# Optimization experiments

Measured on AMD Instinct MI355X. Metric: run time of the kernel, lower is better.

Reference implementation:

```python
import jax, jax.numpy as jnp
import numpy as np
from jax import lax

NPIX = 256        # charge grid size
OS = 3            # oversample / stride
KS = 9            # dynamic kernel window size (3 * OS)
TIME_STEPS = 8
ORDER = 2

# polynomial powers: all (px, py) with px + py <= ORDER, shape (2, n_terms)
_pairs = [(i, s - i) for s in range(ORDER + 1) for i in range(s + 1)]
POWERS = jnp.asarray(np.array(_pairs).T, dtype=jnp.float32)  # (2, 6)
NTERMS = POWERS.shape[1]
NFEAT = 2 * NTERMS  # 12 encoder output channels


def pixel_coords(n, diameter):
    # dLux-style pixel center coordinates, shape (2, n, n)
    pitch = diameter / n
    c = ((jnp.arange(n) - (n - 1) / 2.0) * pitch).astype(jnp.float32)
    return jnp.stack(jnp.meshgrid(c, c, indexing="ij"))


def downsample(x, n, mean):
    h, w = x.shape
    r = x.reshape(h // n, n, w // n, n)
    return r.mean((1, 3)) if mean else r.sum((1, 3))


def conv2d_same(x, w):
    # x: (C, H, W), w: (O, C, 3, 3), SAME padding, no bias
    return lax.conv_general_dilated(
        x[None], w, (1, 1), "SAME",
        dimension_numbers=("NCHW", "OIHW", "NCHW"))[0]


def calc_kernels(coords):
    # coords: (npix, npix, 2, 3, 3) distorted sub-pixel centers
    npix = coords.shape[0]
    # full[c, 3i+p, 3j+q] = coords[i, j, c, p, q]  (kernels_to_array over both channels)
    full = coords.transpose(2, 0, 3, 1, 4).reshape(2, OS * npix, OS * npix)
    pc31 = pixel_coords(3, 1.0)                      # (2, 3, 3)
    empty = jnp.tile(pc31, (1, npix + 2, npix + 2))  # (2, 3(npix+2), 3(npix+2))
    padded = empty.at[:, 3:-3, 3:-3].set(full)
    rel = jnp.repeat(jnp.repeat(pixel_coords(3, 3.0), 3, axis=1), 3, axis=2)  # (2, 9, 9)
    win = jnp.stack([
        jnp.stack([padded[:, u:u + 3 * npix - 2:3, v:v + 3 * npix - 2:3]
                   for v in range(KS)], axis=1)
        for u in range(KS)], axis=1)                 # (2, 9, 9, npix, npix)
    x = win[0] + rel[0][..., None, None]
    y = win[1] + rel[1][..., None, None]
    size = jnp.float32(1.0 / 3.0)
    # overlap of a size x size box at (x, y) with the unit box centered at 0
    ox = jnp.maximum(0.0, jnp.minimum(x + size / 2, 0.5) - jnp.maximum(x - size / 2, -0.5))
    oy = jnp.maximum(0.0, jnp.minimum(y + size / 2, 0.5) - jnp.maximum(y - size / 2, -0.5))
    frac = ox * oy / (size * size)                   # (9, 9, npix, npix)
    return frac.transpose(2, 3, 0, 1)                # (npix, npix, 9, 9)


def dfn_kernels(charge, w1, w2, w3):
    # encoder: conv(1->32) relu conv(32->32) relu conv(32->12)
    f = jax.nn.relu(conv2d_same(charge[None], w1))
    f = jax.nn.relu(conv2d_same(f, w2))
    f = conv2d_same(f, w3)                           # (12, npix, npix)
    npix = charge.shape[-1]
    coeffs = f.reshape(2, NTERMS, npix, npix)        # per-pixel (2, n_terms)
    knots = pixel_coords(3, 1.0)                     # (2, 3, 3)
    pow_base = (knots[0][None] ** POWERS[0][:, None, None]) * \
               (knots[1][None] ** POWERS[1][:, None, None])   # (n_terms, 3, 3)
    distortion = jnp.einsum("ctij,txy->ijcxy", coeffs, pow_base)
    coords = knots[None, None] + distortion          # (npix, npix, 2, 3, 3)
    return calc_kernels(coords)


def apply_kernels_stride(illum, kernels):
    # illum: (3*npix, 3*npix); kernels: (npix, npix, 9, 9)
    npix = kernels.shape[0]
    pad = KS // OS  # 3
    ip = jnp.pad(illum, pad)
    out = jnp.zeros((npix, npix), illum.dtype)
    for u in range(KS):          # fixed 9x9 offset loop, each iter fully vectorized
        for v in range(KS):
            out = out + ip[u:u + 3 * npix - 2:3, v:v + 3 * npix - 2:3] * kernels[:, :, u, v]
    return out


def setup_inputs() -> dict:
    key = jax.random.key(0)
    ks = jax.random.split(key, 6)
    return {
        "bias": jax.random.normal(ks[0], (NPIX, NPIX), jnp.float32),
        "illuminance": jax.random.uniform(ks[1], (3 * NPIX, 3 * NPIX), jnp.float32),
        "sensitivity": jax.random.uniform(ks[2], (3 * NPIX, 3 * NPIX), jnp.float32),
        "w1": 0.05 * jax.random.normal(ks[3], (32, 1, 3, 3), jnp.float32),
        "w2": 0.05 * jax.random.normal(ks[4], (32, 32, 3, 3), jnp.float32),
        "w3": 0.05 * jax.random.normal(ks[5], (NFEAT, 32, 3, 3), jnp.float32),
    }


def reference(bias, illuminance, sensitivity, w1, w2, w3):
    illum_full = illuminance / TIME_STEPS
    illum = downsample(sensitivity * illum_full, OS, mean=False)   # (npix, npix)
    sens = downsample(sensitivity, OS, mean=True)                  # (npix, npix)
    charge = bias - jnp.mean(bias)                                 # use_bias=True
    charges = [charge]
    diffusions = []
    for _ in range(TIME_STEPS):  # bleed=True path
        norm_charge = charge - jnp.mean(charge)
        kernels = dfn_kernels(norm_charge, w1, w2, w3)
        new_charge = sens * apply_kernels_stride(illum_full, kernels)
        charge = charge + new_charge
        diffusions.append(illum - new_charge)
        charges.append(charge)
    ramp = jnp.stack(charges) + jnp.median(bias)                   # (T+1, npix, npix)
    return ramp, jnp.stack(diffusions)                             # (T, npix, npix)
```

## Files before the change

kernel.cpp:

```cpp
#include <hip/hip_runtime.h>

#define N2 65536
#define FW 768

#define WS_CHARGE 0
#define WS_ILLUM  (N2)
#define WS_SENS   (2*N2)
#define WS_FEAT2  (3*N2)
#define WS_W1T    (35*N2)
#define WS_W2T    (WS_W1T + 288)
#define WS_W3T    (WS_W2T + 9216)
#define WS_SUMS   (WS_W3T + 3456)
#define WS_BSUM   (WS_SUMS + 9)
#define WS_MEANB  (WS_SUMS + 10)
#define WS_MEDIAN (WS_SUMS + 11)
#define WS_SEL    (WS_SUMS + 12)
#define WS_H2     (WS_SUMS + 16)
#define WS_H3     (WS_H2 + 2048)
#define NCLEAR    (16 + 2048 + 2048)
#define WS_H1     (WS_H3 + 2048)

__device__ __forceinline__ void block_sum_atomic(float v, float* dst){
  #pragma unroll
  for (int o = 32; o > 0; o >>= 1) v += __shfl_down(v, o, 64);
  __shared__ float red[16];
  int lane = threadIdx.x & 63, wid = threadIdx.x >> 6;
  int nw = (int)(blockDim.x >> 6);
  if (lane == 0) red[wid] = v;
  __syncthreads();
  if (threadIdx.x == 0){
    float s = red[0];
    for (int w = 1; w < nw; w++) s += red[w];
    atomicAdd(dst, s);
  }
}

__device__ __forceinline__ unsigned block_scan_u32(unsigned v, unsigned* wsum){
  __syncthreads();
  int lane = threadIdx.x & 63, wid = threadIdx.x >> 6, nw = (int)(blockDim.x >> 6);
  unsigned x = v;
  #pragma unroll
  for (int o = 1; o < 64; o <<= 1){ unsigned y = __shfl_up(x, o, 64); if (lane >= o) x += y; }
  if (lane == 63) wsum[wid] = x;
  __syncthreads();
  if (wid == 0){
    unsigned w = (lane < nw) ? wsum[lane] : 0u;
    #pragma unroll
    for (int o = 1; o < 16; o <<= 1){ unsigned y = __shfl_up(w, o, 64); if (lane >= o) w += y; }
    if (lane < nw) wsum[lane] = w;
  }
  __syncthreads();
  unsigned base = (wid > 0) ? wsum[wid - 1] : 0u;
  return base + x;
}

__device__ __forceinline__ unsigned key_flip(unsigned u){
  return (u & 0x80000000u) ? ~u : (u ^ 0x80000000u);
}

__global__ __launch_bounds__(256) void k_prep(const float* __restrict__ w1,
    const float* __restrict__ w2, const float* __restrict__ w3,
    float* __restrict__ ws){
  int t = blockIdx.x * 256 + threadIdx.x;
  unsigned* z = (unsigned*)(ws + WS_SUMS);
  for (int i = t; i < NCLEAR; i += 2048) z[i] = 0u;
  for (int idx = t; idx < 288; idx += 2048){
    int co = idx / 9, k = idx - co*9;
    ws[WS_W1T + k*32 + co] = w1[idx];
  }
  for (int idx = t; idx < 9216; idx += 2048){
    int co = idx / 288, r = idx - co*288, ci = r / 9, k = r - ci*9;
    ws[WS_W2T + (ci*9 + k)*32 + co] = w2[idx];
  }
  for (int idx = t; idx < 3456; idx += 2048){
    int co = idx / 288, r = idx - co*288, ci = r / 9, k = r - ci*9;
    ws[WS_W3T + (ci*9 + k)*12 + co] = w3[idx];
  }
}

__global__ __launch_bounds__(256) void k_h1(const float* __restrict__ bias,
                                            float* __restrict__ ws){
  __shared__ unsigned h[4096];
  for (int i = threadIdx.x; i < 4096; i += 256) h[i] = 0u;
  __syncthreads();
  float s = 0.f;
  for (int i = blockIdx.x * 256 + threadIdx.x; i < N2; i += 32*256){
    float v = bias[i]; s += v;
    atomicAdd(&h[key_flip(__float_as_uint(v)) >> 20], 1u);
  }
  __syncthreads();
  unsigned* H1 = (unsigned*)(ws + WS_H1) + (blockIdx.x << 12);
  for (int i = threadIdx.x; i < 4096; i += 256) H1[i] = h[i];
  block_sum_atomic(s, ws + WS_BSUM);
}

__global__ __launch_bounds__(1024) void k_s1(float* __restrict__ ws){
  const unsigned* H1 = (const unsigned*)(ws + WS_H1);
  unsigned* sel = (unsigned*)(ws + WS_SEL);
  __shared__ unsigned wssc[16];
  int t = threadIdx.x;
  uint4 hv = make_uint4(0u, 0u, 0u, 0u);
  for (int b = 0; b < 32; b++){
    uint4 v = ((const uint4*)(H1 + (b << 12)))[t];
    hv.x += v.x; hv.y += v.y; hv.z += v.z; hv.w += v.w;
  }
  unsigned c4 = hv.x + hv.y + hv.z + hv.w;
  unsigned cum = block_scan_u32(c4, wssc);
  unsigned before = cum - c4;
  unsigned hh[4] = {hv.x, hv.y, hv.z, hv.w};
  for (int s = 0; s < 2; s++){
    unsigned rank = 32767u + (unsigned)s;
    if (before <= rank && rank < cum){
      unsigned kk = rank - before, acc = 0; unsigned b = 0;
      for (; b < 3; b++){ if (acc + hh[b] > kk) break; acc += hh[b]; }
      sel[s]     = 4u*(unsigned)t + b;
      sel[2 + s] = kk - acc;
    }
  }
  if (t == 0) ws[WS_MEANB] = ws[WS_BSUM] * (1.f / (float)N2);
}

__global__ __launch_bounds__(256) void k_h23(const float* __restrict__ bias,
    float* __restrict__ ws, unsigned* __restrict__ H, int shift){
  const unsigned* sel = (const unsigned*)(ws + WS_SEL);
  unsigned p0 = sel[0], p1 = sel[1];
  for (int i = blockIdx.x * 256 + threadIdx.x; i < N2; i += 64*256){
    unsigned key = key_flip(__float_as_uint(bias[i]));
    unsigned top = key >> (shift + 10);
    unsigned bin = (key >> shift) & 1023u;
    if (top == p0) atomicAdd(&H[bin], 1u);
    if (top == p1) atomicAdd(&H[1024u + bin], 1u);
  }
}

__global__ __launch_bounds__(1024) void k_s23(float* __restrict__ ws,
    const unsigned* __restrict__ H, int final_lvl){
  unsigned* sel = (unsigned*)(ws + WS_SEL);
  __shared__ unsigned wssc[16];
  __shared__ float meds[2];
  int t = threadIdx.x;
  for (int s = 0; s < 2; s++){
    unsigned cc = H[s*1024 + t];
    unsigned rank = sel[2 + s];
    unsigned cum = block_scan_u32(cc, wssc);
    unsigned before = cum - cc;
    if (before <= rank && rank < cum){
      unsigned p = (sel[s] << 10) | (unsigned)t;
      sel[s]     = p;
      sel[2 + s] = rank - before;
      if (final_lvl){
        unsigned u = (p & 0x80000000u) ? (p ^ 0x80000000u) : ~p;
        meds[s] = __uint_as_float(u);
      }
    }
    __syncthreads();
  }
  if (final_lvl && t == 0) ws[WS_MEDIAN] = 0.5f * (meds[0] + meds[1]);
}

__global__ __launch_bounds__(256) void k_init(const float* __restrict__ bias,
    const float* __restrict__ illum, const float* __restrict__ sens,
    float* __restrict__ ws, float* __restrict__ out){
  int pix = blockIdx.x * 256 + threadIdx.x;
  int i = pix >> 8, j = pix & 255;
  float si = 0.f, ss = 0.f;
  #pragma unroll
  for (int p = 0; p < 3; p++)
    #pragma unroll
    for (int q = 0; q < 3; q++){
      float se = sens[(3*i+p)*FW + 3*j+q];
      float il = illum[(3*i+p)*FW + 3*j+q];
      si = fmaf(se, il * 0.125f, si);
      ss += se;
    }
  ws[WS_ILLUM + pix] = si;
  ws[WS_SENS  + pix] = ss * (1.f/9.f);
  float c = bias[pix] - ws[WS_MEANB];
  ws[WS_CHARGE + pix] = c;
  out[pix] = c + ws[WS_MEDIAN];
  block_sum_atomic(c, ws + WS_SUMS + 0);
}

__global__ __launch_bounds__(512) void k_convA(float* __restrict__ ws,
    const float* __restrict__ w1t, const float* __restrict__ w2t, int step){
  __shared__ float chg[400];
  __shared__ float f1[32*360];
  const float* charge = ws + WS_CHARGE;
  const float mean = ws[WS_SUMS + step] * (1.f / (float)N2);
  const int tile = blockIdx.x >> 1;
  const int half = blockIdx.x & 1;
  const int gi0 = (tile >> 4) << 4, gj0 = (tile & 15) << 4;
  const int tid = threadIdx.x;

  if (tid < 400){
    int r = tid / 20, c = tid - r*20;
    int gi = gi0 + r - 2, gj = gj0 + c - 2;
    float v = 0.f;
    if ((unsigned)gi < 256u && (unsigned)gj < 256u) v = charge[(gi<<8) + gj] - mean;
    chg[tid] = v;
  }
  __syncthreads();

  if (tid < 324){
    int r = tid / 18, c = tid - r*18;
    int gi = gi0 + r - 1, gj = gj0 + c - 1;
    float acc[32];
    #pragma unroll
    for (int co = 0; co < 32; co++) acc[co] = 0.f;
    if ((unsigned)gi < 256u && (unsigned)gj < 256u){
      float x[9];
      #pragma unroll
      for (int dy = 0; dy < 3; dy++)
        #pragma unroll
        for (int dx = 0; dx < 3; dx++) x[dy*3+dx] = chg[(r+dy)*20 + c+dx];
      #pragma unroll
      for (int k = 0; k < 9; k++){
        float xv = x[k];
        const float4* wr = (const float4*)(w1t + k*32);
        #pragma unroll
        for (int g = 0; g < 8; g++){
          float4 w4 = wr[g];
          acc[g*4+0] = fmaf(w4.x, xv, acc[g*4+0]);
          acc[g*4+1] = fmaf(w4.y, xv, acc[g*4+1]);
          acc[g*4+2] = fmaf(w4.z, xv, acc[g*4+2]);
          acc[g*4+3] = fmaf(w4.w, xv, acc[g*4+3]);
        }
      }
      #pragma unroll
      for (int co = 0; co < 32; co++) acc[co] = fmaxf(acc[co], 0.f);
    }
    #pragma unroll
    for (int co = 0; co < 32; co++) f1[co*360 + r*20 + c] = acc[co];
  }
  __syncthreads();

  const int lane = tid & 63;
  const int co2 = __builtin_amdgcn_readfirstlane(half*16 + ((tid >> 6) << 1));
  const int ti = lane >> 2, tjc = (lane & 3) << 2;
  float acc[4][2];
  #pragma unroll
  for (int p = 0; p < 4; p++){ acc[p][0] = 0.f; acc[p][1] = 0.f; }

  const float* wb = w2t + co2;
  for (int ci = 0; ci < 32; ci++){
    float xr[3][6];
    #pragma unroll
    for (int dy = 0; dy < 3; dy++){
      const float* rp = f1 + ci*360 + (ti+dy)*20 + tjc;
      float4 a = *(const float4*)rp;
      float2 b = *(const float2*)(rp + 4);
      xr[dy][0] = a.x; xr[dy][1] = a.y; xr[dy][2] = a.z; xr[dy][3] = a.w;
      xr[dy][4] = b.x; xr[dy][5] = b.y;
    }
    const float* wci = wb + ci*288;
    #pragma unroll
    for (int k = 0; k < 9; k++){
      const int dy = k / 3, dx = k - dy*3;
      float2 w2v = *(const float2*)(wci + k*32);
      #pragma unroll
      for (int p = 0; p < 4; p++){
        float xv = xr[dy][p + dx];
        acc[p][0] = fmaf(w2v.x, xv, acc[p][0]);
        acc[p][1] = fmaf(w2v.y, xv, acc[p][1]);
      }
    }
  }
  float* f2 = ws + WS_FEAT2;
  const int prow = ((gi0 + ti) << 8) + gj0 + tjc;
  #pragma unroll
  for (int cc = 0; cc < 2; cc++){
    float4 v;
    v.x = fmaxf(acc[0][cc], 0.f);
    v.y = fmaxf(acc[1][cc], 0.f);
    v.z = fmaxf(acc[2][cc], 0.f);
    v.w = fmaxf(acc[3][cc], 0.f);
    *(float4*)(f2 + (co2 + cc)*N2 + prow) = v;
  }
}

__global__ __launch_bounds__(512) void k_convB(float* __restrict__ ws,
    const float* __restrict__ w3t, const float* __restrict__ illum,
    float* __restrict__ out, int step){
  __shared__ float tile[32*400];
  __shared__ float S[9*324];
  const float* f2 = ws + WS_FEAT2;
  const int gi0 = (blockIdx.x >> 4) << 4, gj0 = (blockIdx.x & 15) << 4;
  const int tid = threadIdx.x;

  for (int idx = tid; idx < 32*400; idx += 512){
    int ci = idx / 400, px = idx - ci*400, r = px / 20, c = px - r*20;
    int gi = gi0 + r - 2, gj = gj0 + c - 2;
    float v = 0.f;
    if ((unsigned)gi < 256u && (unsigned)gj < 256u) v = f2[ci*N2 + (gi<<8) + gj];
    tile[idx] = v;
  }
  __syncthreads();

  if (tid < 324){
    int a = tid / 18, b = tid - a*18;
    int gi = gi0 + a - 1, gj = gj0 + b - 1;
    float Sv[9];
    #pragma unroll
    for (int d = 0; d < 9; d++) Sv[d] = 0.f;
    if ((unsigned)gi < 256u && (unsigned)gj < 256u){
      float cf[12];
      #pragma unroll
      for (int co = 0; co < 12; co++) cf[co] = 0.f;
      for (int ci = 0; ci < 32; ci++){
        float x[9];
        #pragma unroll
        for (int dy = 0; dy < 3; dy++)
          #pragma unroll
          for (int dx = 0; dx < 3; dx++) x[dy*3+dx] = tile[ci*400 + (a+dy)*20 + (b+dx)];
        #pragma unroll
        for (int k = 0; k < 9; k++){
          const float4* wr = (const float4*)(w3t + (ci*9 + k)*12);
          float4 A = wr[0], B = wr[1], C = wr[2];
          float xv = x[k];
          cf[0] = fmaf(A.x, xv, cf[0]);   cf[1] = fmaf(A.y, xv, cf[1]);
          cf[2] = fmaf(A.z, xv, cf[2]);   cf[3] = fmaf(A.w, xv, cf[3]);
          cf[4] = fmaf(B.x, xv, cf[4]);   cf[5] = fmaf(B.y, xv, cf[5]);
          cf[6] = fmaf(B.z, xv, cf[6]);   cf[7] = fmaf(B.w, xv, cf[7]);
          cf[8] = fmaf(C.x, xv, cf[8]);   cf[9] = fmaf(C.y, xv, cf[9]);
          cf[10] = fmaf(C.z, xv, cf[10]); cf[11] = fmaf(C.w, xv, cf[11]);
        }
      }
      const float third = 1.f/3.f, sixth = 1.f/6.f;
      #pragma unroll
      for (int p = 0; p < 3; p++){
        float kx = (p - 1) * third;
        #pragma unroll
        for (int q = 0; q < 3; q++){
          float ky = (q - 1) * third;
          float cx = kx + cf[0] + cf[1]*ky + cf[2]*kx + cf[3]*ky*ky + cf[4]*kx*ky + cf[5]*kx*kx;
          float cy = ky + cf[6] + cf[7]*ky + cf[8]*kx + cf[9]*ky*ky + cf[10]*kx*ky + cf[11]*kx*kx;
          float Ipq = illum[(3*gi+p)*FW + 3*gj+q] * 0.125f;
          float ox[3], oy[3];
          #pragma unroll
          for (int d = 0; d < 3; d++){
            float xx = cx + (float)(d - 1);
            ox[d] = fmaxf(0.f, fminf(xx + sixth, 0.5f) - fmaxf(xx - sixth, -0.5f));
            float yy = cy + (float)(d - 1);
            oy[d] = fmaxf(0.f, fminf(yy + sixth, 0.5f) - fmaxf(yy - sixth, -0.5f));
          }
          #pragma unroll
          for (int d = 0; d < 3; d++){
            float aa = Ipq * ox[d];
            #pragma unroll
            for (int e = 0; e < 3; e++) Sv[d*3+e] = fmaf(aa, oy[e], Sv[d*3+e]);
          }
        }
      }
    }
    #pragma unroll
    for (int d = 0; d < 9; d++) S[d*324 + tid] = Sv[d];
  }
  __syncthreads();

  float chv = 0.f;
  if (tid < 256){
    int ti = tid >> 4, tj = tid & 15;
    float s = 0.f;
    #pragma unroll
    for (int d = 0; d < 3; d++)
      #pragma unroll
      for (int e = 0; e < 3; e++) s += S[(d*3+e)*324 + (ti+d)*18 + tj+e];
    int pix = ((gi0 + ti) << 8) + gj0 + tj;
    float nc = ws[WS_SENS + pix] * (9.f * s);
    float ch = ws[WS_CHARGE + pix] + nc;
    ws[WS_CHARGE + pix] = ch;
    out[(step + 1)*N2 + pix] = ch + ws[WS_MEDIAN];
    out[(9 + step)*N2 + pix] = ws[WS_ILLUM + pix] - nc;
    chv = ch;
  }
  block_sum_atomic(chv, ws + WS_SUMS + step + 1);
}

extern "C" void kernel_launch(void* const* d_in, const int* in_sizes, int n_in,
                              void* d_out, int out_size, void* d_ws, size_t ws_size,
                              hipStream_t stream) {
  (void)in_sizes; (void)n_in; (void)out_size; (void)ws_size;
  const float* bias  = (const float*)d_in[0];
  const float* illum = (const float*)d_in[1];
  const float* sens  = (const float*)d_in[2];
  const float* w1    = (const float*)d_in[3];
  const float* w2    = (const float*)d_in[4];
  const float* w3    = (const float*)d_in[5];
  float* out = (float*)d_out;
  float* ws  = (float*)d_ws;
  unsigned* H2 = (unsigned*)(ws + WS_H2);
  unsigned* H3 = (unsigned*)(ws + WS_H3);

  k_prep<<<8,   256, 0, stream>>>(w1, w2, w3, ws);
  k_h1  <<<32,  256, 0, stream>>>(bias, ws);
  k_s1  <<<1,  1024, 0, stream>>>(ws);
  k_h23 <<<64,  256, 0, stream>>>(bias, ws, H2, 10);
  k_s23 <<<1,  1024, 0, stream>>>(ws, H2, 0);
  k_h23 <<<64,  256, 0, stream>>>(bias, ws, H3, 0);
  k_s23 <<<1,  1024, 0, stream>>>(ws, H3, 1);
  k_init<<<256, 256, 0, stream>>>(bias, illum, sens, ws, out);
  for (int t = 0; t < 8; t++){
    k_convA<<<512, 512, 0, stream>>>(ws, ws + WS_W1T, ws + WS_W2T, t);
    k_convB<<<256, 512, 0, stream>>>(ws, ws + WS_W3T, illum, out, t);
  }
}
```

Baseline: 583.3 us.

## Split convB channel reduction across two thread halves and parallelize histogram merge

k_convB now launches 1024 threads and splits the 32-channel conv3 reduction into two halves of 16 channels. Each half writes partial coefficients to shared memory, and after a barrier they are summed before the kernel-overlap stage. This is meant to double the active threads in the serial per-pixel reduction, at the cost of extra shared memory (about 31KB more), an added sync, and possibly lower occupancy. Separately, the 32-block histogram merge moves from the single-block k_s1 into a new multi-block k_s1red kernel, which adds one launch.

```diff
diff --git a/kernel.cpp b/kernel.cpp
--- a/kernel.cpp
+++ b/kernel.cpp
@@ -19,6 +19,7 @@
 #define WS_H3     (WS_H2 + 2048)
 #define NCLEAR    (16 + 2048 + 2048)
 #define WS_H1     (WS_H3 + 2048)
+#define WS_H1R    (WS_H1 + 32*4096)
 
 __device__ __forceinline__ void block_sum_atomic(float v, float* dst){
   #pragma unroll
@@ -94,16 +95,22 @@
   block_sum_atomic(s, ws + WS_BSUM);
 }
 
+__global__ __launch_bounds__(128) void k_s1red(float* __restrict__ ws){
+  const unsigned* H1 = (const unsigned*)(ws + WS_H1);
+  unsigned* H1R = (unsigned*)(ws + WS_H1R);
+  int bin = blockIdx.x * 128 + threadIdx.x;
+  unsigned s = 0;
+  #pragma unroll 8
+  for (int b = 0; b < 32; b++) s += H1[(b << 12) + bin];
+  H1R[bin] = s;
+}
+
 __global__ __launch_bounds__(1024) void k_s1(float* __restrict__ ws){
-  const unsigned* H1 = (const unsigned*)(ws + WS_H1);
+  const unsigned* H1R = (const unsigned*)(ws + WS_H1R);
   unsigned* sel = (unsigned*)(ws + WS_SEL);
   __shared__ unsigned wssc[16];
   int t = threadIdx.x;
-  uint4 hv = make_uint4(0u, 0u, 0u, 0u);
-  for (int b = 0; b < 32; b++){
-    uint4 v = ((const uint4*)(H1 + (b << 12)))[t];
-    hv.x += v.x; hv.y += v.y; hv.z += v.z; hv.w += v.w;
-  }
+  uint4 hv = ((const uint4*)H1R)[t];
   unsigned c4 = hv.x + hv.y + hv.z + hv.w;
   unsigned cum = block_scan_u32(c4, wssc);
   unsigned before = cum - c4;
@@ -278,16 +285,17 @@
   }
 }
 
-__global__ __launch_bounds__(512) void k_convB(float* __restrict__ ws,
+__global__ __launch_bounds__(1024) void k_convB(float* __restrict__ ws,
     const float* __restrict__ w3t, const float* __restrict__ illum,
     float* __restrict__ out, int step){
   __shared__ float tile[32*400];
+  __shared__ float coef[648*12];
   __shared__ float S[9*324];
   const float* f2 = ws + WS_FEAT2;
   const int gi0 = (blockIdx.x >> 4) << 4, gj0 = (blockIdx.x & 15) << 4;
   const int tid = threadIdx.x;
 
-  for (int idx = tid; idx < 32*400; idx += 512){
+  for (int idx = tid; idx < 32*400; idx += 1024){
     int ci = idx / 400, px = idx - ci*400, r = px / 20, c = px - r*20;
     int gi = gi0 + r - 2, gj = gj0 + c - 2;
     float v = 0.f;
@@ -296,17 +304,17 @@
   }
   __syncthreads();
 
-  if (tid < 324){
-    int a = tid / 18, b = tid - a*18;
+  if (tid < 648){
+    int h = tid >= 324;
+    int px = tid - h*324;
+    int a = px / 18, b = px - a*18;
     int gi = gi0 + a - 1, gj = gj0 + b - 1;
-    float Sv[9];
-    #pragma unroll
-    for (int d = 0; d < 9; d++) Sv[d] = 0.f;
+    float cf[12];
+    #pragma unroll
+    for (int co = 0; co < 12; co++) cf[co] = 0.f;
     if ((unsigned)gi < 256u && (unsigned)gj < 256u){
-      float cf[12];
-      #pragma unroll
-      for (int co = 0; co < 12; co++) cf[co] = 0.f;
-      for (int ci = 0; ci < 32; ci++){
+      int ci0 = h << 4;
+      for (int ci = ci0; ci < ci0 + 16; ci++){
         float x[9];
         #pragma unroll
         for (int dy = 0; dy < 3; dy++)
@@ -325,6 +333,26 @@
           cf[10] = fmaf(C.z, xv, cf[10]); cf[11] = fmaf(C.w, xv, cf[11]);
         }
       }
+    }
+    float* cp = coef + tid*12;
+    *(float4*)(cp)     = make_float4(cf[0], cf[1], cf[2], cf[3]);
+    *(float4*)(cp + 4) = make_float4(cf[4], cf[5], cf[6], cf[7]);
+    *(float4*)(cp + 8) = make_float4(cf[8], cf[9], cf[10], cf[11]);
+  }
+  __syncthreads();
+
+  if (tid < 324){
+    int a = tid / 18, b = tid - a*18;
+    int gi = gi0 + a - 1, gj = gj0 + b - 1;
+    float Sv[9];
+    #pragma unroll
+    for (int d = 0; d < 9; d++) Sv[d] = 0.f;
+    if ((unsigned)gi < 256u && (unsigned)gj < 256u){
+      const float* c0 = coef + tid*12;
+      const float* c1 = coef + (324 + tid)*12;
+      float cf[12];
+      #pragma unroll
+      for (int co = 0; co < 12; co++) cf[co] = c0[co] + c1[co];
       const float third = 1.f/3.f, sixth = 1.f/6.f;
       #pragma unroll
       for (int p = 0; p < 3; p++){
@@ -391,16 +419,17 @@
   unsigned* H2 = (unsigned*)(ws + WS_H2);
   unsigned* H3 = (unsigned*)(ws + WS_H3);
 
-  k_prep<<<8,   256, 0, stream>>>(w1, w2, w3, ws);
-  k_h1  <<<32,  256, 0, stream>>>(bias, ws);
-  k_s1  <<<1,  1024, 0, stream>>>(ws);
-  k_h23 <<<64,  256, 0, stream>>>(bias, ws, H2, 10);
-  k_s23 <<<1,  1024, 0, stream>>>(ws, H2, 0);
-  k_h23 <<<64,  256, 0, stream>>>(bias, ws, H3, 0);
-  k_s23 <<<1,  1024, 0, stream>>>(ws, H3, 1);
-  k_init<<<256, 256, 0, stream>>>(bias, illum, sens, ws, out);
+  k_prep <<<8,   256, 0, stream>>>(w1, w2, w3, ws);
+  k_h1   <<<32,  256, 0, stream>>>(bias, ws);
+  k_s1red<<<32,  128, 0, stream>>>(ws);
+  k_s1   <<<1,  1024, 0, stream>>>(ws);
+  k_h23  <<<64,  256, 0, stream>>>(bias, ws, H2, 10);
+  k_s23  <<<1,  1024, 0, stream>>>(ws, H2, 0);
+  k_h23  <<<64,  256, 0, stream>>>(bias, ws, H3, 0);
+  k_s23  <<<1,  1024, 0, stream>>>(ws, H3, 1);
+  k_init <<<256, 256, 0, stream>>>(bias, illum, sens, ws, out);
   for (int t = 0; t < 8; t++){
     k_convA<<<512, 512, 0, stream>>>(ws, ws + WS_W1T, ws + WS_W2T, t);
-    k_convB<<<256, 512, 0, stream>>>(ws, ws + WS_W3T, illum, out, t);
-  }
-}
+    k_convB<<<256, 1024, 0, stream>>>(ws, ws + WS_W3T, illum, out, t);
+  }
+}
```

Result: slower. 675.3 us (+15.8%).
